# Kernel optimization log

Hardware: AMD Instinct MI355X
Metric: run time of the kernel (lower is better)

## Reference

```python
import jax, jax.numpy as jnp
import numpy as np

HIDDEN = 1024
NUM_HEADS = 16
HEAD_DIM = HIDDEN // NUM_HEADS  # 64
MLP_HIDDEN = 4096
RMS_EPS = 1e-6


def setup_inputs() -> dict:
    key = jax.random.key(0)
    ks = jax.random.split(key, 4)
    B, L = 2, 2048
    x = jax.random.normal(ks[0], (B, L, HIDDEN), dtype=jnp.float32)
    pe = jax.random.normal(ks[1], (1, 1, L, HEAD_DIM // 2, 2, 2), dtype=jnp.float32)
    W1 = jax.random.normal(ks[2], (HIDDEN, 3 * HIDDEN + MLP_HIDDEN), dtype=jnp.float32) * (HIDDEN ** -0.5)
    b1 = jnp.zeros((3 * HIDDEN + MLP_HIDDEN,), dtype=jnp.float32)
    W2 = jax.random.normal(ks[3], (HIDDEN + MLP_HIDDEN, HIDDEN), dtype=jnp.float32) * ((HIDDEN + MLP_HIDDEN) ** -0.5)
    b2 = jnp.zeros((HIDDEN,), dtype=jnp.float32)
    q_scale = jnp.ones((HEAD_DIM,), dtype=jnp.float32)
    k_scale = jnp.ones((HEAD_DIM,), dtype=jnp.float32)
    return {"x": x, "pe": pe, "W1": W1, "b1": b1, "W2": W2, "b2": b2,
            "q_scale": q_scale, "k_scale": k_scale}


def _rms_norm(t, scale):
    # RMSNorm over last dim (head_dim) with learnable scale (flux QKNorm)
    rrms = jax.lax.rsqrt(jnp.mean(jnp.square(t), axis=-1, keepdims=True) + RMS_EPS)
    return t * rrms * scale


def _apply_rope(xq, xk, pe):
    # pe: [1,1,L,D/2,2,2]; x*: [B,H,L,D]
    def rope(t):
        t_ = t.reshape(*t.shape[:-1], -1, 1, 2)  # [B,H,L,D/2,1,2]
        out = pe[..., 0] * t_[..., 0] + pe[..., 1] * t_[..., 1]  # [B,H,L,D/2,2]
        return out.reshape(*t.shape)
    return rope(xq), rope(xk)


def reference(x, pe, W1, b1, W2, b2, q_scale, k_scale):
    B, L, _ = x.shape
    h = x @ W1 + b1  # [B,L,3H+Mh]
    qkv, mlp = h[..., : 3 * HIDDEN], h[..., 3 * HIDDEN:]
    # 'B L (K H D) -> K B H L D'
    qkv = qkv.reshape(B, L, 3, NUM_HEADS, HEAD_DIM).transpose(2, 0, 3, 1, 4)
    q, k, v = qkv[0], qkv[1], qkv[2]
    q = _rms_norm(q, q_scale)
    k = _rms_norm(k, k_scale)
    q, k = _apply_rope(q, k, pe)
    scale = HEAD_DIM ** -0.5
    scores = jnp.einsum('bhqd,bhkd->bhqk', q, k) * scale
    attn = jnp.einsum('bhqk,bhkd->bhqd', jax.nn.softmax(scores, axis=-1), v)
    attn = attn.transpose(0, 2, 1, 3).reshape(B, L, HIDDEN)  # 'B H L D -> B L (H D)'
    out = jnp.concatenate((attn, jax.nn.gelu(mlp)), axis=2) @ W2 + b2
    return out
```

## Files before the change

### kernel.cpp

```cpp
#include <hip/hip_runtime.h>

typedef __bf16 bf16;
typedef __bf16 bf16x8 __attribute__((ext_vector_type(8)));
typedef float f32x4 __attribute__((ext_vector_type(4)));
typedef float f32x16 __attribute__((ext_vector_type(16)));

#define GLDS16(gp, lp) __builtin_amdgcn_global_load_lds( \
    (__attribute__((address_space(1))) void*)(gp), \
    (__attribute__((address_space(3))) void*)(lp), 16, 0, 0)

__device__ inline float ex2(float x) { return exp2f(x); }

__device__ inline float gelu_fast(float x) {
    float t = ex2(-2.3022081702f * (x + 0.044715f * x * x * x));
    return x * __builtin_amdgcn_rcpf(1.0f + t);
}


__global__ void f2b_kernel(const float* __restrict__ src, bf16* __restrict__ dst, long n) {
    long i = ((long)blockIdx.x * 256 + threadIdx.x) * 4;
    if (i + 3 < n) {
        float4 v = *(const float4*)&src[i];
        dst[i + 0] = (bf16)v.x;
        dst[i + 1] = (bf16)v.y;
        dst[i + 2] = (bf16)v.z;
        dst[i + 3] = (bf16)v.w;
    }
}

__global__ __launch_bounds__(256) void transpose_f2b(const float* __restrict__ W,
                                                     bf16* __restrict__ WT,
                                                     int K, int N) {
    __shared__ float tile[32][33];
    int tx = threadIdx.x & 31;
    int ty = threadIdx.x >> 5;
    int n0 = blockIdx.x * 32;
    int k0 = blockIdx.y * 32;
#pragma unroll
    for (int i = 0; i < 4; ++i)
        tile[ty + i * 8][tx] = W[(long)(k0 + ty + i * 8) * N + n0 + tx];
    __syncthreads();
#pragma unroll
    for (int i = 0; i < 4; ++i)
        WT[(long)(n0 + ty + i * 8) * K + k0 + tx] = (bf16)tile[tx][ty + i * 8];
}

template <int EPI>
__global__ __launch_bounds__(256) void gemm_bt(const bf16* __restrict__ A,
                                               const bf16* __restrict__ BT,
                                               const float* __restrict__ bias,
                                               void* __restrict__ C0,
                                               void* __restrict__ C1,
                                               int M, int N, int K, int kch) {
    __shared__ __align__(16) char Asm[128 * 128];
    __shared__ __align__(16) char Bsm[128 * 128];
    int tid = threadIdx.x;
    int w = tid >> 6, l = tid & 63;
    int wr = w >> 1, wc = w & 1;
    int bm = blockIdx.x * 128;
    int bn = blockIdx.y * 128;
    int k0base = (EPI == 1) ? blockIdx.z * kch : 0;

    f32x4 acc[4][4] = {};

    int fr = l & 15;
    int g16 = (l >> 4) * 16;
    int xsw = (fr & 7) << 4;

    int srow = tid >> 3;
    int sg8 = ((tid & 7) ^ (srow & 7)) * 8;
    int dstoff = (w << 10) + ((l & 63) << 4);

    int nk = kch >> 6;
    for (int kt = 0; kt < nk; ++kt) {
        int k0 = k0base + kt * 64;
#pragma unroll
        for (int gg = 0; gg < 4; ++gg) {
            const bf16* ga = A + (long)(bm + gg * 32 + srow) * K + k0 + sg8;
            GLDS16(ga, Asm + gg * 4096 + dstoff);
            const bf16* gb = BT + (long)(bn + gg * 32 + srow) * K + k0 + sg8;
            GLDS16(gb, Bsm + gg * 4096 + dstoff);
        }
        asm volatile("s_waitcnt vmcnt(0)" ::: "memory");
        __syncthreads();

#pragma unroll
        for (int kk = 0; kk < 2; ++kk) {
            int koff = (kk * 64 + g16) ^ xsw;
            bf16x8 af[4], bfr[4];
#pragma unroll
            for (int m = 0; m < 4; ++m)
                af[m] = *(const bf16x8*)(Asm + (wr * 64 + m * 16 + fr) * 128 + koff);
#pragma unroll
            for (int n = 0; n < 4; ++n)
                bfr[n] = *(const bf16x8*)(Bsm + (wc * 64 + n * 16 + fr) * 128 + koff);
#pragma unroll
            for (int m = 0; m < 4; ++m)
#pragma unroll
                for (int n = 0; n < 4; ++n)
                    acc[m][n] = __builtin_amdgcn_mfma_f32_16x16x32_bf16(af[m], bfr[n], acc[m][n], 0, 0, 0);
        }
        __syncthreads();
    }

    int orow0 = bm + wr * 64;
    int ocol0 = bn + wc * 64;
    if (EPI == 0) {
        bf16* hp = (bf16*)C0;
        bf16* cat = (bf16*)C1;
        bool gel = (bn >= 3072);
#pragma unroll
        for (int m = 0; m < 4; ++m) {
            int row = orow0 + m * 16 + (l >> 4) * 4;
#pragma unroll
            for (int n = 0; n < 4; ++n) {
                int col = ocol0 + n * 16 + fr;
                float bv = bias[col];
#pragma unroll
                for (int r = 0; r < 4; ++r) {
                    float v = acc[m][n][r] + bv;
                    if (gel) {
                        cat[(long)(row + r) * 5120 + 1024 + col - 3072] = (bf16)gelu_fast(v);
                    } else {
                        hp[(long)(row + r) * N + col] = (bf16)v;
                    }
                }
            }
        }
    } else {
        float* cz = (float*)C0 + (long)blockIdx.z * M * N;
#pragma unroll
        for (int m = 0; m < 4; ++m) {
            int row = orow0 + m * 16 + (l >> 4) * 4;
#pragma unroll
            for (int n = 0; n < 4; ++n) {
                int col = ocol0 + n * 16 + fr;
#pragma unroll
                for (int r = 0; r < 4; ++r)
                    cz[(long)(row + r) * N + col] = acc[m][n][r];
            }
        }
    }
}

__global__ __launch_bounds__(256) void reduce4_kernel(const float* __restrict__ part,
                                                      const float* __restrict__ b2,
                                                      float* __restrict__ out) {
    const long stride4 = 4096L * 1024 / 4;
#pragma unroll
    for (int it = 0; it < 2; ++it) {
        long i4 = (long)blockIdx.x * 512 + it * 256 + threadIdx.x;
        float4 s = *(const float4*)&b2[(i4 * 4) & 1023];
        const float4* p = (const float4*)part;
#pragma unroll
        for (int z = 0; z < 4; ++z) {
            float4 v = p[z * stride4 + i4];
            s.x += v.x; s.y += v.y; s.z += v.z; s.w += v.w;
        }
        *(float4*)&out[i4 * 4] = s;
    }
}

__global__ __launch_bounds__(256) void qkv_kernel(const bf16* __restrict__ h,
                                                  const float* __restrict__ pe,
                                                  const float* __restrict__ qsc_,
                                                  const float* __restrict__ ksc_,
                                                  bf16* __restrict__ qo,
                                                  bf16* __restrict__ ko) {
    int t = blockIdx.x;
    int b = t >> 11;
    int lpos = t & 2047;
    int wv = threadIdx.x >> 6;
    int d = threadIdx.x & 63;
    const bf16* hrow = h + (long)t * 7168;
    float pe0 = pe[lpos * 128 + (d >> 1) * 4 + (d & 1) * 2 + 0];
    float pe1 = pe[lpos * 128 + (d >> 1) * 4 + (d & 1) * 2 + 1];
    float qsc = qsc_[d], ksc = ksc_[d];
#pragma unroll 1
    for (int it = 0; it < 4; ++it) {
        int hh = wv * 4 + it;
        float qv = (float)hrow[hh * 64 + d];
        float kv = (float)hrow[1024 + hh * 64 + d];
        float ssq = qv * qv, ssk = kv * kv;
#pragma unroll
        for (int off = 1; off < 64; off <<= 1) {
            ssq += __shfl_xor(ssq, off, 64);
            ssk += __shfl_xor(ssk, off, 64);
        }
        float qn = qv * rsqrtf(ssq * (1.0f / 64.0f) + 1e-6f) * qsc;
        float kn = kv * rsqrtf(ssk * (1.0f / 64.0f) + 1e-6f) * ksc;
        float qe = __shfl(qn, d & 62, 64), qodd = __shfl(qn, d | 1, 64);
        float ke = __shfl(kn, d & 62, 64), kodd = __shfl(kn, d | 1, 64);
        float qr = (pe0 * qe + pe1 * qodd) * 0.18033688011112042f;
        float kr = pe0 * ke + pe1 * kodd;
        long base = ((long)(b * 16 + hh) * 2048 + lpos) * 64 + d;
        qo[base] = (bf16)qr;
        ko[base] = (bf16)kr;
    }
}

__global__ __launch_bounds__(256) void vtrans_kernel(const bf16* __restrict__ h,
                                                     bf16* __restrict__ vT) {
    __shared__ unsigned short tile[64 * 65];
    int bh = blockIdx.x;
    int b = bh >> 4, hh = bh & 15;
    int l0 = blockIdx.y * 64;
    int tid = threadIdx.x;

    int r = tid >> 3, c = tid & 7;
#pragma unroll
    for (int p = 0; p < 2; ++p) {
        int row = r + p * 32;
        const bf16* src = h + (long)(b * 2048 + l0 + row) * 7168 + 2048 + hh * 64 + c * 8;
        bf16x8 v = *(const bf16x8*)src;
        union { bf16x8 v; unsigned short s[8]; } u; u.v = v;
#pragma unroll
        for (int e = 0; e < 8; ++e) tile[row * 65 + c * 8 + e] = u.s[e];
    }
    __syncthreads();
#pragma unroll
    for (int p = 0; p < 2; ++p) {
        int idx = tid + p * 256;
        int d = idx >> 3, kg = idx & 7;
        union { bf16x8 v; unsigned short s[8]; } u;
#pragma unroll
        for (int e = 0; e < 8; ++e) u.s[e] = tile[(kg * 8 + e) * 65 + d];
        *(bf16x8*)&vT[((long)bh * 64 + d) * 2048 + l0 + kg * 8] = u.v;
    }
}

__global__ __launch_bounds__(256) void attn_kernel(const bf16* __restrict__ qg,
                                                   const bf16* __restrict__ kg_,
                                                   const bf16* __restrict__ vT,
                                                   bf16* __restrict__ cat) {
    __shared__ __align__(16) char lds[49152];
    char* Kl0 = lds;
    char* Kl1 = lds + 8192;
    char* Vl0 = lds + 16384;
    char* Vl1 = lds + 24576;

    int bidx = blockIdx.x;
    int bh = bidx & 31;
    int qblk = bidx >> 5;
    int b = bh >> 4, hh = bh & 15;
    int tid = threadIdx.x;
    int wv = tid >> 6, l = tid & 63;
    int h = l >> 5, ln = l & 31;
    int sw = (ln & 7) << 4;

    char* Pw = lds + 32768 + wv * 4096;

    const bf16* qbase = qg + ((long)bh * 2048 + qblk * 128 + wv * 32 + ln) * 64 + h * 8;
    bf16x8 qf[4];
#pragma unroll
    for (int ds = 0; ds < 4; ++ds) qf[ds] = *(const bf16x8*)(qbase + ds * 16);

    f32x16 Oa0 = {}, Oa1 = {};
    float m = -1e30f, lsum = 0.0f;

    int kr = tid >> 3, kg = tid & 7;
    int swb = (kg * 16) ^ ((kr & 7) << 4);
    const bf16* gK = kg_ + ((long)bh * 2048 + kr) * 64 + kg * 8;
    const bf16* gV = vT + ((long)bh * 64 + kr) * 2048 + kg * 8;

    bf16x8 rk0 = *(const bf16x8*)gK;
    bf16x8 rk1 = *(const bf16x8*)(gK + 32 * 64);
    bf16x8 rv0 = *(const bf16x8*)gV;
    bf16x8 rv1 = *(const bf16x8*)(gV + 32 * 2048);
    *(bf16x8*)(Kl0 + kr * 128 + swb) = rk0;
    *(bf16x8*)(Kl0 + (kr + 32) * 128 + swb) = rk1;
    *(bf16x8*)(Vl0 + kr * 128 + swb) = rv0;
    *(bf16x8*)(Vl0 + (kr + 32) * 128 + swb) = rv1;
    __syncthreads();

    int c = 0;
    for (int t = 0; t < 32; ++t) {
        if (t < 31) {
            rk0 = *(const bf16x8*)(gK + (long)(t + 1) * 4096);
            rk1 = *(const bf16x8*)(gK + (long)(t + 1) * 4096 + 32 * 64);
            rv0 = *(const bf16x8*)(gV + (t + 1) * 64);
            rv1 = *(const bf16x8*)(gV + (t + 1) * 64 + 32 * 2048);
        }
        const char* Kc = c ? Kl1 : Kl0;
        const char* Vc = c ? Vl1 : Vl0;

        f32x16 S0 = {}, S1 = {};
        __builtin_amdgcn_s_setprio(1);
#pragma unroll
        for (int ds = 0; ds < 4; ++ds) {
            bf16x8 kf0 = *(const bf16x8*)(Kc + ln * 128 + ((ds * 32 + h * 16) ^ sw));
            bf16x8 kf1 = *(const bf16x8*)(Kc + (32 + ln) * 128 + ((ds * 32 + h * 16) ^ sw));
            S0 = __builtin_amdgcn_mfma_f32_32x32x16_bf16(kf0, qf[ds], S0, 0, 0, 0);
            S1 = __builtin_amdgcn_mfma_f32_32x32x16_bf16(kf1, qf[ds], S1, 0, 0, 0);
        }
        __builtin_amdgcn_s_setprio(0);

        float tmax = S0[0];
#pragma unroll
        for (int r = 1; r < 16; ++r) tmax = fmaxf(tmax, S0[r]);
#pragma unroll
        for (int r = 0; r < 16; ++r) tmax = fmaxf(tmax, S1[r]);
        tmax = fmaxf(tmax, __shfl_xor(tmax, 32, 64));

        if (!__all(tmax - m <= 8.0f)) {
            float mn = fmaxf(m, tmax);
            float es = ex2(m - mn);
            lsum *= es;
            m = mn;
#pragma unroll
            for (int r = 0; r < 16; ++r) {
                int rowq = (r & 3) + 8 * (r >> 2) + 4 * h;
                float esr = __shfl(es, rowq, 64);
                Oa0[r] *= esr;
                Oa1[r] *= esr;
            }
        }

        float ps = 0.0f;
#pragma unroll
        for (int kvt = 0; kvt < 2; ++kvt) {
            float p[16];
#pragma unroll
            for (int r = 0; r < 16; ++r) {
                float v = ex2((kvt ? S1[r] : S0[r]) - m);
                p[r] = v;
                ps += v;
            }
#pragma unroll
            for (int i = 0; i < 8; ++i) {
                union { bf16 bb[2]; unsigned u; } pr;
                pr.bb[0] = (bf16)p[2 * i];
                pr.bb[1] = (bf16)p[2 * i + 1];
                int kv = ((2 * i) & 3) + 8 * (i >> 1) + 4 * h + 32 * kvt;
                *(unsigned*)(Pw + ln * 128 + ((kv * 2) ^ sw)) = pr.u;
            }
        }
        lsum += ps + __shfl_xor(ps, 32, 64);

        asm volatile("s_waitcnt lgkmcnt(0)" ::: "memory");

        bf16x8 pa[4];
#pragma unroll
        for (int s = 0; s < 4; ++s)
            pa[s] = *(const bf16x8*)(Pw + ln * 128 + ((s * 32 + h * 16) ^ sw));

        __builtin_amdgcn_s_setprio(1);
#pragma unroll
        for (int s = 0; s < 4; ++s) {
            bf16x8 vf0 = *(const bf16x8*)(Vc + ln * 128 + ((s * 32 + h * 16) ^ sw));
            bf16x8 vf1 = *(const bf16x8*)(Vc + (32 + ln) * 128 + ((s * 32 + h * 16) ^ sw));
            Oa0 = __builtin_amdgcn_mfma_f32_32x32x16_bf16(pa[s], vf0, Oa0, 0, 0, 0);
            Oa1 = __builtin_amdgcn_mfma_f32_32x32x16_bf16(pa[s], vf1, Oa1, 0, 0, 0);
        }
        __builtin_amdgcn_s_setprio(0);

        __syncthreads();
        if (t < 31) {
            char* Kn = c ? Kl0 : Kl1;
            char* Vn = c ? Vl0 : Vl1;
            *(bf16x8*)(Kn + kr * 128 + swb) = rk0;
            *(bf16x8*)(Kn + (kr + 32) * 128 + swb) = rk1;
            *(bf16x8*)(Vn + kr * 128 + swb) = rv0;
            *(bf16x8*)(Vn + (kr + 32) * 128 + swb) = rv1;
        }
        __syncthreads();
        c ^= 1;
    }

#pragma unroll
    for (int r = 0; r < 16; ++r) {
        int rowq = (r & 3) + 8 * (r >> 2) + 4 * h;
        float ls = __shfl(lsum, rowq, 64);
        float inv = 1.0f / ls;
        long trow = (long)b * 2048 + qblk * 128 + wv * 32 + rowq;
        cat[trow * 5120 + hh * 64 + ln] = (bf16)(Oa0[r] * inv);
        cat[trow * 5120 + hh * 64 + 32 + ln] = (bf16)(Oa1[r] * inv);
    }
}


extern "C" void kernel_launch(void* const* d_in, const int* in_sizes, int n_in,
                              void* d_out, int out_size, void* d_ws, size_t ws_size,
                              hipStream_t stream) {
    const float* x  = (const float*)d_in[0];
    const float* pe = (const float*)d_in[1];
    const float* W1 = (const float*)d_in[2];
    const float* b1 = (const float*)d_in[3];
    const float* W2 = (const float*)d_in[4];
    const float* b2 = (const float*)d_in[5];
    const float* qs = (const float*)d_in[6];
    const float* ks = (const float*)d_in[7];
    float* out = (float*)d_out;

    char* ws = (char*)d_ws;
    bf16* xb  = (bf16*)(ws);
    bf16* w1t = (bf16*)(ws + 8388608);
    bf16* w2t = (bf16*)(ws + 23068672);
    bf16* h   = (bf16*)(ws + 33554432);
    bf16* qb  = (bf16*)(ws + 92274688);
    bf16* kb  = (bf16*)(ws + 100663296);
    bf16* vT  = (bf16*)(ws + 109051904);
    bf16* cat = (bf16*)(ws + 117440512);
    float* part = (float*)(ws + 33554432);

    f2b_kernel<<<4096, 256, 0, stream>>>(x, xb, 4194304L);
    transpose_f2b<<<dim3(224, 32), 256, 0, stream>>>(W1, w1t, 1024, 7168);
    transpose_f2b<<<dim3(32, 160), 256, 0, stream>>>(W2, w2t, 5120, 1024);

    gemm_bt<0><<<dim3(32, 56), 256, 0, stream>>>(xb, w1t, b1, h, cat, 4096, 7168, 1024, 1024);

    qkv_kernel<<<4096, 256, 0, stream>>>(h, pe, qs, ks, qb, kb);
    vtrans_kernel<<<dim3(32, 32), 256, 0, stream>>>(h, vT);

    attn_kernel<<<512, 256, 0, stream>>>(qb, kb, vT, cat);

    gemm_bt<1><<<dim3(32, 8, 4), 256, 0, stream>>>(cat, w2t, nullptr, part, nullptr, 4096, 1024, 5120, 1280);
    reduce4_kernel<<<2048, 256, 0, stream>>>(part, b2, out);
}
```

Before: 273.8 us.

## Replace GEMM with 256x256 tile, 8-wave double-buffered pipelined kernel

```diff
diff --git a/kernel.cpp b/kernel.cpp
--- a/kernel.cpp
+++ b/kernel.cpp
@@ -45,80 +45,109 @@
         WT[(long)(n0 + ty + i * 8) * K + k0 + tx] = (bf16)tile[tx][ty + i * 8];
 }
 
+#define STA(tile, ch) if ((tile) < NT) { \
+    const bf16* s_ = gA + (tile) * 64 + (ch) * 32; \
+    char* d_ = lds + ((tile) & 1) * 65536 + (ch) * 16384 + tid * 16; \
+    GLDS16(s_, d_); GLDS16(s_ + (long)128 * K, d_ + 8192); }
+
+#define STB(tile, ch) if ((tile) < NT) { \
+    const bf16* s_ = gB + (tile) * 64 + (ch) * 32; \
+    char* d_ = lds + ((tile) & 1) * 65536 + 32768 + (ch) * 16384 + tid * 16; \
+    GLDS16(s_, d_); GLDS16(s_ + (long)128 * K, d_ + 8192); }
+
+#define PH(tb, mh, kh, RB, STAGE_STMT, WAITN) do { \
+    STAGE_STMT; \
+    asm volatile("s_waitcnt vmcnt(" #WAITN ")" ::: "memory"); \
+    asm volatile("s_barrier" ::: "memory"); \
+    { const char* Ab_ = lds + (tb) * 65536 + (kh) * 16384; \
+      const char* Bb_ = lds + (tb) * 65536 + 32768 + (kh) * 16384; \
+      if (RB) { \
+        _Pragma("unroll") for (int n_ = 0; n_ < 4; ++n_) \
+          bfrag[n_] = *(const bf16x8*)(Bb_ + (wc * 64 + n_ * 16 + fr) * 64 + aslot); } \
+      bf16x8 af_[4]; \
+      _Pragma("unroll") for (int i_ = 0; i_ < 4; ++i_) \
+          af_[i_] = *(const bf16x8*)(Ab_ + (wr * 128 + (mh) * 64 + i_ * 16 + fr) * 64 + aslot); \
+      __builtin_amdgcn_s_setprio(1); \
+      _Pragma("unroll") for (int n_ = 0; n_ < 4; ++n_) \
+        _Pragma("unroll") for (int i_ = 0; i_ < 4; ++i_) \
+          acc[(mh) * 4 + i_][n_] = __builtin_amdgcn_mfma_f32_16x16x32_bf16(af_[i_], bfrag[n_], acc[(mh) * 4 + i_][n_], 0, 0, 0); \
+      __builtin_amdgcn_s_setprio(0); \
+    } \
+    asm volatile("s_barrier" ::: "memory"); \
+} while (0)
+
 template <int EPI>
-__global__ __launch_bounds__(256) void gemm_bt(const bf16* __restrict__ A,
-                                               const bf16* __restrict__ BT,
-                                               const float* __restrict__ bias,
-                                               void* __restrict__ C0,
-                                               void* __restrict__ C1,
-                                               int M, int N, int K, int kch) {
-    __shared__ __align__(16) char Asm[128 * 128];
-    __shared__ __align__(16) char Bsm[128 * 128];
+__global__ __launch_bounds__(512, 2) void gemm8p(const bf16* __restrict__ A_,
+                                                 const bf16* __restrict__ BT_,
+                                                 const float* __restrict__ bias,
+                                                 void* __restrict__ C0,
+                                                 void* __restrict__ C1,
+                                                 int M, int N, int K, int kch) {
+    __shared__ __align__(16) char lds[131072];
+
+    int bx, by, k0base = 0;
+    if (EPI == 0) {
+        int bid = blockIdx.x;
+        int swz = (bid & 7) * 56 + (bid >> 3);
+        bx = swz % 16; by = swz / 16;
+    } else {
+        bx = blockIdx.x; by = blockIdx.y;
+        k0base = blockIdx.z * kch;
+    }
+    int bm = bx * 256, bn = by * 256;
+    int NT = kch >> 6;
+
     int tid = threadIdx.x;
     int w = tid >> 6, l = tid & 63;
-    int wr = w >> 1, wc = w & 1;
-    int bm = blockIdx.x * 128;
-    int bn = blockIdx.y * 128;
-    int k0base = (EPI == 1) ? blockIdx.z * kch : 0;
-
-    f32x4 acc[4][4] = {};
-
+    int wr = w >> 2, wc = w & 3;
     int fr = l & 15;
-    int g16 = (l >> 4) * 16;
-    int xsw = (fr & 7) << 4;
-
-    int srow = tid >> 3;
-    int sg8 = ((tid & 7) ^ (srow & 7)) * 8;
-    int dstoff = (w << 10) + ((l & 63) << 4);
-
-    int nk = kch >> 6;
-    for (int kt = 0; kt < nk; ++kt) {
-        int k0 = k0base + kt * 64;
-#pragma unroll
-        for (int gg = 0; gg < 4; ++gg) {
-            const bf16* ga = A + (long)(bm + gg * 32 + srow) * K + k0 + sg8;
-            GLDS16(ga, Asm + gg * 4096 + dstoff);
-            const bf16* gb = BT + (long)(bn + gg * 32 + srow) * K + k0 + sg8;
-            GLDS16(gb, Bsm + gg * 4096 + dstoff);
-        }
-        asm volatile("s_waitcnt vmcnt(0)" ::: "memory");
-        __syncthreads();
-
-#pragma unroll
-        for (int kk = 0; kk < 2; ++kk) {
-            int koff = (kk * 64 + g16) ^ xsw;
-            bf16x8 af[4], bfr[4];
-#pragma unroll
-            for (int m = 0; m < 4; ++m)
-                af[m] = *(const bf16x8*)(Asm + (wr * 64 + m * 16 + fr) * 128 + koff);
-#pragma unroll
-            for (int n = 0; n < 4; ++n)
-                bfr[n] = *(const bf16x8*)(Bsm + (wc * 64 + n * 16 + fr) * 128 + koff);
-#pragma unroll
-            for (int m = 0; m < 4; ++m)
-#pragma unroll
-                for (int n = 0; n < 4; ++n)
-                    acc[m][n] = __builtin_amdgcn_mfma_f32_16x16x32_bf16(af[m], bfr[n], acc[m][n], 0, 0, 0);
-        }
-        __syncthreads();
-    }
-
-    int orow0 = bm + wr * 64;
-    int ocol0 = bn + wc * 64;
+    int aslot = (((l >> 4) ^ ((fr >> 1) & 3)) << 4);
+
+    int srow0 = tid >> 2;
+    int sgoff = (((tid & 3) ^ ((srow0 >> 1) & 3)) << 3);
+    const bf16* gA = A_ + (long)(bm + srow0) * K + k0base + sgoff;
+    const bf16* gB = BT_ + (long)(bn + srow0) * K + k0base + sgoff;
+
+    f32x4 acc[8][4] = {};
+    bf16x8 bfrag[4];
+
+    STA(0, 0); STA(0, 1); STB(0, 0); STB(0, 1);
+    STB(1, 0); STA(1, 0); STB(1, 1);
+    asm volatile("s_waitcnt vmcnt(0)" ::: "memory");
+    asm volatile("s_barrier" ::: "memory");
+
+    int NI = NT >> 1;
+    for (int i = 0; i < NI; ++i) {
+        int t1 = 2 * i + 1, t2 = 2 * i + 2, t3 = 2 * i + 3;
+        if (i == NI - 1) {
+            PH(0, 0, 0, true, STA(t1, 1), 0);
+        } else {
+            PH(0, 0, 0, true, STA(t1, 1), 12);
+        }
+        PH(0, 1, 0, false, STB(t2, 0), 12);
+        PH(0, 0, 1, true,  STA(t2, 0), 12);
+        PH(0, 1, 1, false, STB(t2, 1), 12);
+        PH(1, 0, 0, true,  STA(t2, 1), 12);
+        PH(1, 1, 0, false, STB(t3, 0), 12);
+        PH(1, 0, 1, true,  STA(t3, 0), 12);
+        PH(1, 1, 1, false, STB(t3, 1), 12);
+    }
+
+    int r4 = (l >> 4) * 4;
     if (EPI == 0) {
         bf16* hp = (bf16*)C0;
         bf16* cat = (bf16*)C1;
         bool gel = (bn >= 3072);
 #pragma unroll
-        for (int m = 0; m < 4; ++m) {
-            int row = orow0 + m * 16 + (l >> 4) * 4;
+        for (int mi = 0; mi < 8; ++mi) {
+            int row = bm + wr * 128 + mi * 16 + r4;
 #pragma unroll
             for (int n = 0; n < 4; ++n) {
-                int col = ocol0 + n * 16 + fr;
+                int col = bn + wc * 64 + n * 16 + fr;
                 float bv = bias[col];
 #pragma unroll
                 for (int r = 0; r < 4; ++r) {
-                    float v = acc[m][n][r] + bv;
+                    float v = acc[mi][n][r] + bv;
                     if (gel) {
                         cat[(long)(row + r) * 5120 + 1024 + col - 3072] = (bf16)gelu_fast(v);
                     } else {
@@ -130,14 +159,14 @@
     } else {
         float* cz = (float*)C0 + (long)blockIdx.z * M * N;
 #pragma unroll
-        for (int m = 0; m < 4; ++m) {
-            int row = orow0 + m * 16 + (l >> 4) * 4;
+        for (int mi = 0; mi < 8; ++mi) {
+            int row = bm + wr * 128 + mi * 16 + r4;
 #pragma unroll
             for (int n = 0; n < 4; ++n) {
-                int col = ocol0 + n * 16 + fr;
+                int col = bn + wc * 64 + n * 16 + fr;
 #pragma unroll
                 for (int r = 0; r < 4; ++r)
-                    cz[(long)(row + r) * N + col] = acc[m][n][r];
+                    cz[(long)(row + r) * N + col] = acc[mi][n][r];
             }
         }
     }
@@ -407,13 +436,13 @@
     transpose_f2b<<<dim3(224, 32), 256, 0, stream>>>(W1, w1t, 1024, 7168);
     transpose_f2b<<<dim3(32, 160), 256, 0, stream>>>(W2, w2t, 5120, 1024);
 
-    gemm_bt<0><<<dim3(32, 56), 256, 0, stream>>>(xb, w1t, b1, h, cat, 4096, 7168, 1024, 1024);
+    gemm8p<0><<<dim3(448), 512, 0, stream>>>(xb, w1t, b1, h, cat, 4096, 7168, 1024, 1024);
 
     qkv_kernel<<<4096, 256, 0, stream>>>(h, pe, qs, ks, qb, kb);
     vtrans_kernel<<<dim3(32, 32), 256, 0, stream>>>(h, vT);
 
     attn_kernel<<<512, 256, 0, stream>>>(qb, kb, vT, cat);
 
-    gemm_bt<1><<<dim3(32, 8, 4), 256, 0, stream>>>(cat, w2t, nullptr, part, nullptr, 4096, 1024, 5120, 1280);
+    gemm8p<1><<<dim3(16, 4, 4), 512, 0, stream>>>(cat, w2t, nullptr, part, nullptr, 4096, 1024, 5120, 1280);
     reduce4_kernel<<<2048, 256, 0, stream>>>(part, b2, out);
 }
```

Measured after the change: 265.6 us. 3.0% less time.
